# Optimization experiments

Hardware: AMD Instinct MI355X
Metric: run time of the kernel (lower is better)

## Reference

```python
import jax, jax.numpy as jnp
import numpy as np

B, D, K = 16384, 4096, 14
EPS = 1e-12  # torch F.normalize eps


def _normalize(x):
    n = jnp.sqrt(jnp.sum(x * x, axis=-1, keepdims=True))
    return x / jnp.maximum(n, EPS)


def setup_inputs() -> dict:
    key = jax.random.key(0)
    ks = jax.random.split(key, 9)
    image_feat = jax.random.normal(ks[0], (B, D), dtype=jnp.float32)
    text_feat = jax.random.normal(ks[1], (B, D), dtype=jnp.float32)
    disease_labels = jax.random.randint(ks[2], (B, K), 0, 2, dtype=jnp.int32)
    # nn.Linear default init: U(-1/sqrt(D), 1/sqrt(D))
    lim = 1.0 / np.sqrt(D)
    Wv = jax.random.uniform(ks[3], (D, D), jnp.float32, -lim, lim)
    bv = jax.random.uniform(ks[4], (D,), jnp.float32, -lim, lim)
    Wt = jax.random.uniform(ks[5], (D, D), jnp.float32, -lim, lim)
    bt = jax.random.uniform(ks[6], (D,), jnp.float32, -lim, lim)
    prototypes = jax.random.normal(ks[7], (K, D), dtype=jnp.float32) * 0.02
    cooccur = np.eye(K, dtype=np.float32)
    for i, j in [(1, 3), (0, 9), (7, 9)]:
        cooccur[i, j] = 0.7
        cooccur[j, i] = 0.7
    cooccurrence = jnp.asarray(cooccur)
    return {
        "image_feat": image_feat, "text_feat": text_feat,
        "disease_labels": disease_labels,
        "Wv": Wv, "bv": bv, "Wt": Wt, "bt": bt,
        "prototypes": prototypes, "cooccurrence": cooccurrence,
    }


def reference(image_feat, text_feat, disease_labels, Wv, bv, Wt, bt, prototypes, cooccurrence):
    labels_f = disease_labels.astype(jnp.float32)  # [B, K]
    v = _normalize(image_feat @ Wv.T + bv)          # [B, D]
    t = _normalize(text_feat @ Wt.T + bt)           # [B, D]
    p = _normalize(prototypes)                      # [K, D]
    v_sim = v @ p.T                                 # [B, K]
    t_sim = t @ p.T                                 # [B, K]
    # Coalition value is linear in the mask and the sampled coalitions differ
    # only at index i, so every Monte Carlo marginal equals this closed form
    # exactly (randomness cancels in value_with - value_without).
    shapley = 0.5 * (v_sim + t_sim) * labels_f      # [B, K]
    batch_cooccur = (labels_f.T @ labels_f) / labels_f.shape[0]  # [K, K]
    learned = jax.nn.sigmoid(cooccurrence)
    cooccur_loss = jnp.mean((learned - jax.lax.stop_gradient(batch_cooccur)) ** 2)
    return shapley, prototypes, cooccur_loss
```

## Files before the change

kernel.cpp:

```cpp
#include <hip/hip_runtime.h>

typedef __bf16 bf16x8 __attribute__((ext_vector_type(8)));
typedef float f32x4 __attribute__((ext_vector_type(4)));
typedef unsigned short u16;
typedef unsigned int u32;

#define D_DIM 4096
#define B_ROWS 16384
#define K_CLS 14
#define M_TOT 32768

__device__ __forceinline__ u32 f2bf(float f) {
    u32 u = __float_as_uint(f);
    return (u + 0x7FFFu + ((u >> 16) & 1u)) >> 16;
}
__device__ __forceinline__ float bfl(u32 u) { return __uint_as_float(u << 16); }
__device__ __forceinline__ float bfh(u32 u) { return __uint_as_float(u & 0xFFFF0000u); }

typedef __attribute__((address_space(3))) void lds_void;
typedef __attribute__((address_space(1))) void glb_void;

__device__ __forceinline__ void g2lds16(const void* g, void* l) {
    __builtin_amdgcn_global_load_lds(
        reinterpret_cast<glb_void*>(reinterpret_cast<uintptr_t>(g)),
        reinterpret_cast<lds_void*>(reinterpret_cast<uintptr_t>(l)),
        16, 0, 0);
}

__global__ void cast_bf16(const float* __restrict__ src, u16* __restrict__ dst, int n4) {
    int i = blockIdx.x * blockDim.x + threadIdx.x;
    int stride = gridDim.x * blockDim.x;
    for (; i < n4; i += stride) {
        float4 a = ((const float4*)src)[i];
        uint2 o;
        o.x = f2bf(a.x) | (f2bf(a.y) << 16);
        o.y = f2bf(a.z) | (f2bf(a.w) << 16);
        ((uint2*)dst)[i] = o;
    }
}

__global__ void proto_norm(const float* __restrict__ P, u16* __restrict__ pTbf,
                           float* __restrict__ outProto) {
    const int k = blockIdx.x;
    const int tid = threadIdx.x;
    float ss = 0.f;
    for (int d = tid; d < D_DIM; d += 256) {
        float v = P[k * D_DIM + d];
        ss += v * v;
    }
    for (int off = 32; off; off >>= 1) ss += __shfl_down(ss, off);
    __shared__ float red[4];
    if ((tid & 63) == 0) red[tid >> 6] = ss;
    __syncthreads();
    float tot = red[0] + red[1] + red[2] + red[3];
    float inv = 1.0f / fmaxf(sqrtf(tot), 1e-12f);
    for (int d = tid; d < D_DIM; d += 256) {
        float v = P[k * D_DIM + d];
        outProto[k * D_DIM + d] = v;
        pTbf[(size_t)d * 16 + k] = (u16)f2bf(v * inv);
    }
}

__global__ void cooccur_bc(const int* __restrict__ L, float* __restrict__ bc) {
    const int i = blockIdx.x / K_CLS, j = blockIdx.x % K_CLS;
    int s = 0;
    for (int b = threadIdx.x; b < B_ROWS; b += 256)
        s += L[b * K_CLS + i] * L[b * K_CLS + j];
    for (int off = 32; off; off >>= 1) s += __shfl_down(s, off);
    __shared__ int red[4];
    if ((threadIdx.x & 63) == 0) red[threadIdx.x >> 6] = s;
    __syncthreads();
    if (threadIdx.x == 0)
        bc[blockIdx.x] = (float)(red[0] + red[1] + red[2] + red[3]) / (float)B_ROWS;
}

__global__ void cooccur_loss(const float* __restrict__ C, const float* __restrict__ bc,
                             float* __restrict__ out) {
    const int t = threadIdx.x;
    float d2 = 0.f;
    if (t < K_CLS * K_CLS) {
        float s = 1.0f / (1.0f + expf(-C[t]));
        float d = s - bc[t];
        d2 = d * d;
    }
    for (int off = 32; off; off >>= 1) d2 += __shfl_down(d2, off);
    __shared__ float red[4];
    if ((t & 63) == 0) red[t >> 6] = d2;
    __syncthreads();
    if (t == 0) out[0] = (red[0] + red[1] + red[2] + red[3]) / (float)(K_CLS * K_CLS);
}

#define BK 64
#define NKT (D_DIM / BK)
#define TILE_E (256 * 64)

#define STAGE(ABUF, BBUF, k0) do {                                             \
    _Pragma("unroll")                                                          \
    for (int i_ = 0; i_ < 4; i_++)                                             \
        g2lds16(Apan + gOff[i_] + (k0), (ABUF) + lOff[i_]);                    \
    _Pragma("unroll")                                                          \
    for (int i_ = 0; i_ < 4; i_++)                                             \
        g2lds16(Bpan + gOff[i_] + (k0), (BBUF) + lOff[i_]);                    \
} while (0)

#define LOAD_B(BBUF) do {                                                      \
    _Pragma("unroll")                                                          \
    for (int ni_ = 0; ni_ < 4; ni_++) {                                        \
        bfr[ni_][0] = *(const bf16x8*)((BBUF) + bBase + ni_ * 16 * BK + so0);  \
        bfr[ni_][1] = *(const bf16x8*)((BBUF) + bBase + ni_ * 16 * BK + so1);  \
    }                                                                          \
} while (0)

#define LOAD_A(ABUF, q) do {                                                   \
    _Pragma("unroll")                                                          \
    for (int s_ = 0; s_ < 2; s_++) {                                           \
        afr[s_][0] = *(const bf16x8*)((ABUF) + aBase + ((q) * 32 + s_ * 16) * BK + so0); \
        afr[s_][1] = *(const bf16x8*)((ABUF) + aBase + ((q) * 32 + s_ * 16) * BK + so1); \
    }                                                                          \
} while (0)

#define MFMA_PHASE(q) do {                                                     \
    __builtin_amdgcn_s_setprio(1);                                             \
    _Pragma("unroll")                                                          \
    for (int s_ = 0; s_ < 2; s_++)                                             \
    _Pragma("unroll")                                                          \
    for (int ni_ = 0; ni_ < 4; ni_++) {                                        \
        acc[(q) * 2 + s_][ni_] = __builtin_amdgcn_mfma_f32_16x16x32_bf16(      \
            afr[s_][0], bfr[ni_][0], acc[(q) * 2 + s_][ni_], 0, 0, 0);         \
        acc[(q) * 2 + s_][ni_] = __builtin_amdgcn_mfma_f32_16x16x32_bf16(      \
            afr[s_][1], bfr[ni_][1], acc[(q) * 2 + s_][ni_], 0, 0, 0);         \
    }                                                                          \
    __builtin_amdgcn_s_setprio(0);                                             \
} while (0)

#define PHASE0(ABUF, BBUF) do { LOAD_B(BBUF); LOAD_A(ABUF, 0);                 \
    __builtin_amdgcn_s_barrier();                                              \
    asm volatile("s_waitcnt lgkmcnt(0)" ::: "memory");                         \
    __builtin_amdgcn_sched_barrier(0);                                         \
    MFMA_PHASE(0);                                                             \
    __builtin_amdgcn_s_barrier(); } while (0)

#define PHASEQ(ABUF, q) do { LOAD_A(ABUF, q);                                  \
    __builtin_amdgcn_s_barrier();                                              \
    asm volatile("s_waitcnt lgkmcnt(0)" ::: "memory");                         \
    __builtin_amdgcn_sched_barrier(0);                                         \
    MFMA_PHASE(q);                                                             \
    __builtin_amdgcn_s_barrier(); } while (0)

#define TILE_BODY(ABUF, BBUF, t) do {                                          \
    bf16x8 bfr[4][2], afr[2][2];                                               \
    PHASE0(ABUF, BBUF);                                                        \
    PHASEQ(ABUF, 1);                                                           \
    PHASEQ(ABUF, 2);                                                           \
    PHASEQ(ABUF, 3);                                                           \
    __builtin_amdgcn_sched_barrier(0);                                         \
    if ((t) + 2 < NKT) {                                                       \
        STAGE(ABUF, BBUF, ((t) + 2) * BK);                                     \
        asm volatile("s_waitcnt vmcnt(8)" ::: "memory");                       \
    } else if ((t) + 1 < NKT) {                                                \
        asm volatile("s_waitcnt vmcnt(0)" ::: "memory");                       \
    }                                                                          \
    __builtin_amdgcn_sched_barrier(0);                                         \
    __builtin_amdgcn_s_barrier();                                              \
} while (0)

__global__ __launch_bounds__(512, 2) void gemm_bt(
    const u16* __restrict__ Xbf,
    const u16* __restrict__ Wbf,
    const float* __restrict__ bv, const float* __restrict__ bt,
    u16* __restrict__ Ybf)
{
    __shared__ __align__(16) u16 lds[4 * TILE_E];
    u16* const As0 = lds;
    u16* const As1 = lds + TILE_E;
    u16* const Bs0 = lds + 2 * TILE_E;
    u16* const Bs1 = lds + 3 * TILE_E;

    const int tid = threadIdx.x;
    const int wave = tid >> 6, lane = tid & 63;

    const int bid = blockIdx.x;
    const int swzb = (bid & 7) * 256 + (bid >> 3);
    const int bn0 = (swzb & 15) * 256;
    const int bm0 = (swzb >> 4) * 256;
    const int half = (bm0 >= B_ROWS) ? 1 : 0;
    const u16* __restrict__ Apan = Xbf + (size_t)bm0 * D_DIM;
    const u16* __restrict__ Bpan = Wbf + (size_t)half * D_DIM * D_DIM
                                       + (size_t)bn0 * D_DIM;
    const float* bias = half ? bt : bv;

    const int lrow = lane >> 3;
    const int lslot = ((lane & 7) ^ lrow) * 8;
    size_t gOff[4];
    int lOff[4];
#pragma unroll
    for (int i = 0; i < 4; i++) {
        const int c = wave * 4 + i;
        gOff[i] = (size_t)(c * 8 + lrow) * D_DIM + lslot;
        lOff[i] = c * 512;
    }

    const int wm = wave >> 2, wn = wave & 3;
    const int mlane = lane & 15, quad = lane >> 4;
    const int lswz = lane & 7;
    const int so0 = (quad ^ lswz) * 8;
    const int so1 = ((4 + quad) ^ lswz) * 8;
    const int aBase = (wm * 128 + mlane) * BK;
    const int bBase = (wn * 64 + mlane) * BK;

    f32x4 acc[8][4] = {};

    STAGE(As0, Bs0, 0);
    STAGE(As1, Bs1, BK);
    asm volatile("s_waitcnt vmcnt(8)" ::: "memory");
    __builtin_amdgcn_sched_barrier(0);
    __builtin_amdgcn_s_barrier();

    for (int tt = 0; tt < NKT; tt += 2) {
        TILE_BODY(As0, Bs0, tt);
        TILE_BODY(As1, Bs1, tt + 1);
    }

#pragma unroll
    for (int ni = 0; ni < 4; ni++) {
        const int col = bn0 + wn * 64 + ni * 16 + mlane;
        const float bcol = bias[col];
#pragma unroll
        for (int mi = 0; mi < 8; mi++) {
            f32x4 v = acc[mi][ni];
            const size_t rb = (size_t)(bm0 + wm * 128 + mi * 16 + quad * 4) * D_DIM + col;
#pragma unroll
            for (int r = 0; r < 4; r++)
                Ybf[rb + (size_t)r * D_DIM] = (u16)f2bf(v[r] + bcol);
        }
    }
}

__global__ __launch_bounds__(256) void simproj(
    const u16* __restrict__ Ybf, const u16* __restrict__ pTbf,
    const int* __restrict__ L, float* __restrict__ out)
{
    const int tid = threadIdx.x;
    const int wave = tid >> 6, lane = tid & 63;
    const int r0 = blockIdx.x * 8 + wave * 2;
    const u16* Yi = Ybf + (size_t)r0 * D_DIM;
    const u16* Yt = Yi + (size_t)B_ROWS * D_DIM;

    float acc[4][15];
#pragma unroll
    for (int r = 0; r < 4; r++)
#pragma unroll
        for (int k = 0; k < 15; k++) acc[r][k] = 0.f;

#pragma unroll 2
    for (int i = 0; i < 64; i++) {
        const int d = lane + i * 64;
        const uint4* pq = (const uint4*)(pTbf + (size_t)d * 16);
        const uint4 q0 = pq[0], q1 = pq[1];
        const float p[14] = { bfl(q0.x), bfh(q0.x), bfl(q0.y), bfh(q0.y),
                              bfl(q0.z), bfh(q0.z), bfl(q0.w), bfh(q0.w),
                              bfl(q1.x), bfh(q1.x), bfl(q1.y), bfh(q1.y),
                              bfl(q1.z), bfh(q1.z) };
        float yv[4];
        yv[0] = bfl((u32)Yi[d]);
        yv[1] = bfl((u32)Yi[D_DIM + d]);
        yv[2] = bfl((u32)Yt[d]);
        yv[3] = bfl((u32)Yt[D_DIM + d]);
#pragma unroll
        for (int r = 0; r < 4; r++) {
            acc[r][14] += yv[r] * yv[r];
#pragma unroll
            for (int k = 0; k < 14; k++) acc[r][k] += yv[r] * p[k];
        }
    }
#pragma unroll
    for (int r = 0; r < 4; r++)
#pragma unroll
        for (int k = 0; k < 15; k++) {
            float v = acc[r][k];
            v += __shfl_xor(v, 1);  v += __shfl_xor(v, 2);  v += __shfl_xor(v, 4);
            v += __shfl_xor(v, 8);  v += __shfl_xor(v, 16); v += __shfl_xor(v, 32);
            acc[r][k] = v;
        }
    if (lane == 0) {
#pragma unroll
        for (int rr = 0; rr < 2; rr++) {
            const float iv = 1.0f / fmaxf(sqrtf(acc[rr][14]), 1e-12f);
            const float it = 1.0f / fmaxf(sqrtf(acc[2 + rr][14]), 1e-12f);
#pragma unroll
            for (int k = 0; k < 14; k++) {
                const int idx = (r0 + rr) * K_CLS + k;
                out[idx] = 0.5f * (acc[rr][k] * iv + acc[2 + rr][k] * it)
                           * (float)L[idx];
            }
        }
    }
}

extern "C" void kernel_launch(void* const* d_in, const int* in_sizes, int n_in,
                              void* d_out, int out_size, void* d_ws, size_t ws_size,
                              hipStream_t stream) {
    const float* image  = (const float*)d_in[0];
    const float* text   = (const float*)d_in[1];
    const int*   labels = (const int*)d_in[2];
    const float* Wv     = (const float*)d_in[3];
    const float* bv     = (const float*)d_in[4];
    const float* Wt     = (const float*)d_in[5];
    const float* bt     = (const float*)d_in[6];
    const float* protos = (const float*)d_in[7];
    const float* cooc   = (const float*)d_in[8];
    float* out = (float*)d_out;

    const size_t OFF_X   = 0;
    const size_t OFF_W   = 268435456ull;
    const size_t OFF_Y   = 335544320ull;
    const size_t OFF_PT  = 603979776ull;
    const size_t OFF_SIM = 604110848ull;
    const size_t OFF_BC  = 605945856ull;
    const size_t NEED    = 605946640ull;
    if (ws_size < NEED) return;
    (void)OFF_SIM;

    char* ws = (char*)d_ws;
    u16*   Xbf  = (u16*)(ws + OFF_X);
    u16*   Wbf  = (u16*)(ws + OFF_W);
    u16*   Ybf  = (u16*)(ws + OFF_Y);
    u16*   pTbf = (u16*)(ws + OFF_PT);
    float* bc   = (float*)(ws + OFF_BC);

    cast_bf16<<<4096, 256, 0, stream>>>(image, Xbf, (B_ROWS * D_DIM) / 4);
    cast_bf16<<<4096, 256, 0, stream>>>(text, Xbf + (size_t)B_ROWS * D_DIM, (B_ROWS * D_DIM) / 4);
    cast_bf16<<<2048, 256, 0, stream>>>(Wv, Wbf, (D_DIM * D_DIM) / 4);
    cast_bf16<<<2048, 256, 0, stream>>>(Wt, Wbf + (size_t)D_DIM * D_DIM, (D_DIM * D_DIM) / 4);

    proto_norm<<<K_CLS, 256, 0, stream>>>(protos, pTbf, out + B_ROWS * K_CLS);
    cooccur_bc<<<K_CLS * K_CLS, 256, 0, stream>>>(labels, bc);
    cooccur_loss<<<1, 256, 0, stream>>>(cooc, bc, out + B_ROWS * K_CLS + K_CLS * D_DIM);

    gemm_bt<<<(M_TOT / 256) * (D_DIM / 256), 512, 0, stream>>>(Xbf, Wbf, bv, bt, Ybf);

    simproj<<<B_ROWS / 8, 256, 0, stream>>>(Ybf, pTbf, labels, out);
}
```

Measured before the change: 1.888 ms.

## Interleave half-tile staging into GEMM phases, remap blocks, merge casts, widen simproj

The GEMM now issues half-tile global-to-LDS loads inside each MFMA phase, spreading the prefetch across the loop instead of doing one block per tile. The wave-to-row mapping and the XCD block mapping change so that each XCD covers contiguous M panels. The four cast launches become a single kernel, and simproj loads 8-wide vectors for 4 rows per wave to reuse each prototype load across more rows. These changes cut launch overhead and idle time waiting on loads, at the cost of more register pressure in simproj and more delicate vmcnt accounting.

```diff
diff --git a/kernel.cpp b/kernel.cpp
--- a/kernel.cpp
+++ b/kernel.cpp
@@ -27,15 +27,25 @@
         16, 0, 0);
 }
 
-__global__ void cast_bf16(const float* __restrict__ src, u16* __restrict__ dst, int n4) {
+__global__ void cast_all(const float* __restrict__ im, const float* __restrict__ tx,
+                         const float* __restrict__ wv, const float* __restrict__ wt,
+                         u16* __restrict__ Xbf, u16* __restrict__ Wbf) {
+    const int nX = (B_ROWS * D_DIM) / 4;
+    const int nW = (D_DIM * D_DIM) / 4;
+    const int total = 2 * nX + 2 * nW;
     int i = blockIdx.x * blockDim.x + threadIdx.x;
-    int stride = gridDim.x * blockDim.x;
-    for (; i < n4; i += stride) {
-        float4 a = ((const float4*)src)[i];
+    const int stride = gridDim.x * blockDim.x;
+    for (; i < total; i += stride) {
+        const float* s; u16* d; int off;
+        if (i < nX)               { s = im; d = Xbf;                       off = i; }
+        else if (i < 2 * nX)      { s = tx; d = Xbf + (size_t)nX * 4;      off = i - nX; }
+        else if (i < 2 * nX + nW) { s = wv; d = Wbf;                       off = i - 2 * nX; }
+        else                      { s = wt; d = Wbf + (size_t)nW * 4;      off = i - 2 * nX - nW; }
+        float4 a = ((const float4*)s)[off];
         uint2 o;
         o.x = f2bf(a.x) | (f2bf(a.y) << 16);
         o.y = f2bf(a.z) | (f2bf(a.w) << 16);
-        ((uint2*)dst)[i] = o;
+        ((uint2*)d)[off] = o;
     }
 }
 
@@ -94,28 +104,28 @@
 #define NKT (D_DIM / BK)
 #define TILE_E (256 * 64)
 
-#define STAGE(ABUF, BBUF, k0) do {                                             \
-    _Pragma("unroll")                                                          \
-    for (int i_ = 0; i_ < 4; i_++)                                             \
-        g2lds16(Apan + gOff[i_] + (k0), (ABUF) + lOff[i_]);                    \
-    _Pragma("unroll")                                                          \
-    for (int i_ = 0; i_ < 4; i_++)                                             \
-        g2lds16(Bpan + gOff[i_] + (k0), (BBUF) + lOff[i_]);                    \
-} while (0)
-
-#define LOAD_B(BBUF) do {                                                      \
+#define STAGE_HALF(DST, PAN, k0, h) do {                                       \
+    _Pragma("unroll")                                                          \
+    for (int i_ = 0; i_ < 2; i_++) {                                           \
+        const int c_ = (h) * 16 + wave * 2 + i_;                               \
+        g2lds16((PAN) + (size_t)(c_ * 8 + lrow) * D_DIM + lslot + (k0),        \
+                (DST) + c_ * 512);                                             \
+    }                                                                          \
+} while (0)
+
+#define LOAD_B(BR) do {                                                        \
     _Pragma("unroll")                                                          \
     for (int ni_ = 0; ni_ < 4; ni_++) {                                        \
-        bfr[ni_][0] = *(const bf16x8*)((BBUF) + bBase + ni_ * 16 * BK + so0);  \
-        bfr[ni_][1] = *(const bf16x8*)((BBUF) + bBase + ni_ * 16 * BK + so1);  \
+        bfr[ni_][0] = *(const bf16x8*)((BR) + bBase + ni_ * 16 * BK + so0);    \
+        bfr[ni_][1] = *(const bf16x8*)((BR) + bBase + ni_ * 16 * BK + so1);    \
     }                                                                          \
 } while (0)
 
-#define LOAD_A(ABUF, q) do {                                                   \
+#define LOAD_A(AR, q) do {                                                     \
     _Pragma("unroll")                                                          \
     for (int s_ = 0; s_ < 2; s_++) {                                           \
-        afr[s_][0] = *(const bf16x8*)((ABUF) + aBase + ((q) * 32 + s_ * 16) * BK + so0); \
-        afr[s_][1] = *(const bf16x8*)((ABUF) + aBase + ((q) * 32 + s_ * 16) * BK + so1); \
+        afr[s_][0] = *(const bf16x8*)((AR) + aBase + ((q) * 64 + s_ * 16) * BK + so0); \
+        afr[s_][1] = *(const bf16x8*)((AR) + aBase + ((q) * 64 + s_ * 16) * BK + so1); \
     }                                                                          \
 } while (0)
 
@@ -133,36 +143,20 @@
     __builtin_amdgcn_s_setprio(0);                                             \
 } while (0)
 
-#define PHASE0(ABUF, BBUF) do { LOAD_B(BBUF); LOAD_A(ABUF, 0);                 \
-    __builtin_amdgcn_s_barrier();                                              \
-    asm volatile("s_waitcnt lgkmcnt(0)" ::: "memory");                         \
+#define PHASE(AR, BR, q, WITHB, STAGE_STMT, TAIL_STMT) do {                    \
+    if (WITHB) { LOAD_B(BR); }                                                 \
+    LOAD_A(AR, q);                                                             \
+    STAGE_STMT;                                                                \
     __builtin_amdgcn_sched_barrier(0);                                         \
-    MFMA_PHASE(0);                                                             \
-    __builtin_amdgcn_s_barrier(); } while (0)
-
-#define PHASEQ(ABUF, q) do { LOAD_A(ABUF, q);                                  \
     __builtin_amdgcn_s_barrier();                                              \
     asm volatile("s_waitcnt lgkmcnt(0)" ::: "memory");                         \
     __builtin_amdgcn_sched_barrier(0);                                         \
     MFMA_PHASE(q);                                                             \
-    __builtin_amdgcn_s_barrier(); } while (0)
-
-#define TILE_BODY(ABUF, BBUF, t) do {                                          \
-    bf16x8 bfr[4][2], afr[2][2];                                               \
-    PHASE0(ABUF, BBUF);                                                        \
-    PHASEQ(ABUF, 1);                                                           \
-    PHASEQ(ABUF, 2);                                                           \
-    PHASEQ(ABUF, 3);                                                           \
-    __builtin_amdgcn_sched_barrier(0);                                         \
-    if ((t) + 2 < NKT) {                                                       \
-        STAGE(ABUF, BBUF, ((t) + 2) * BK);                                     \
-        asm volatile("s_waitcnt vmcnt(8)" ::: "memory");                       \
-    } else if ((t) + 1 < NKT) {                                                \
-        asm volatile("s_waitcnt vmcnt(0)" ::: "memory");                       \
-    }                                                                          \
-    __builtin_amdgcn_sched_barrier(0);                                         \
+    TAIL_STMT;                                                                 \
     __builtin_amdgcn_s_barrier();                                              \
 } while (0)
+
+#define WAIT2 asm volatile("s_waitcnt vmcnt(2)" ::: "memory")
 
 __global__ __launch_bounds__(512, 2) void gemm_bt(
     const u16* __restrict__ Xbf,
@@ -180,9 +174,9 @@
     const int wave = tid >> 6, lane = tid & 63;
 
     const int bid = blockIdx.x;
-    const int swzb = (bid & 7) * 256 + (bid >> 3);
-    const int bn0 = (swzb & 15) * 256;
-    const int bm0 = (swzb >> 4) * 256;
+    const int xcd = bid & 7, loc = bid >> 3;
+    const int bn0 = (loc >> 4) * 256;
+    const int bm0 = (xcd * 16 + (loc & 15)) * 256;
     const int half = (bm0 >= B_ROWS) ? 1 : 0;
     const u16* __restrict__ Apan = Xbf + (size_t)bm0 * D_DIM;
     const u16* __restrict__ Bpan = Wbf + (size_t)half * D_DIM * D_DIM
@@ -191,35 +185,41 @@
 
     const int lrow = lane >> 3;
     const int lslot = ((lane & 7) ^ lrow) * 8;
-    size_t gOff[4];
-    int lOff[4];
-#pragma unroll
-    for (int i = 0; i < 4; i++) {
-        const int c = wave * 4 + i;
-        gOff[i] = (size_t)(c * 8 + lrow) * D_DIM + lslot;
-        lOff[i] = c * 512;
-    }
 
     const int wm = wave >> 2, wn = wave & 3;
     const int mlane = lane & 15, quad = lane >> 4;
     const int lswz = lane & 7;
     const int so0 = (quad ^ lswz) * 8;
     const int so1 = ((4 + quad) ^ lswz) * 8;
-    const int aBase = (wm * 128 + mlane) * BK;
+    const int aBase = (wm * 32 + mlane) * BK;
     const int bBase = (wn * 64 + mlane) * BK;
 
     f32x4 acc[8][4] = {};
 
-    STAGE(As0, Bs0, 0);
-    STAGE(As1, Bs1, BK);
-    asm volatile("s_waitcnt vmcnt(8)" ::: "memory");
+    STAGE_HALF(As0, Apan, 0, 0);
+    STAGE_HALF(As0, Apan, 0, 1);
+    STAGE_HALF(Bs0, Bpan, 0, 0);
+    STAGE_HALF(Bs0, Bpan, 0, 1);
+    STAGE_HALF(As1, Apan, BK, 0);
+    WAIT2;
     __builtin_amdgcn_sched_barrier(0);
     __builtin_amdgcn_s_barrier();
 
     for (int tt = 0; tt < NKT; tt += 2) {
-        TILE_BODY(As0, Bs0, tt);
-        TILE_BODY(As1, Bs1, tt + 1);
-    }
+        const int k1 = (tt + 1) * BK;
+        const int k2 = (tt + 2) * BK;
+        const int k3 = (tt + 3) * BK;
+        bf16x8 bfr[4][2], afr[2][2];
+        PHASE(As0, Bs0, 0, 1, STAGE_HALF(As1, Apan, k1, 1), );
+        PHASE(As0, Bs0, 1, 0, STAGE_HALF(Bs1, Bpan, k1, 0), );
+        PHASE(As0, Bs0, 2, 0, STAGE_HALF(Bs1, Bpan, k1, 1), );
+        PHASE(As0, Bs0, 3, 0, STAGE_HALF(As0, Apan, k2, 0), WAIT2);
+        PHASE(As1, Bs1, 0, 1, STAGE_HALF(As0, Apan, k2, 1), );
+        PHASE(As1, Bs1, 1, 0, STAGE_HALF(Bs0, Bpan, k2, 0), );
+        PHASE(As1, Bs1, 2, 0, STAGE_HALF(Bs0, Bpan, k2, 1), );
+        PHASE(As1, Bs1, 3, 0, STAGE_HALF(As1, Apan, k3, 0), WAIT2);
+    }
+    asm volatile("s_waitcnt vmcnt(0)" ::: "memory");
 
 #pragma unroll
     for (int ni = 0; ni < 4; ni++) {
@@ -228,7 +228,8 @@
 #pragma unroll
         for (int mi = 0; mi < 8; mi++) {
             f32x4 v = acc[mi][ni];
-            const size_t rb = (size_t)(bm0 + wm * 128 + mi * 16 + quad * 4) * D_DIM + col;
+            const int row0 = bm0 + (mi >> 1) * 64 + wm * 32 + (mi & 1) * 16 + quad * 4;
+            const size_t rb = (size_t)row0 * D_DIM + col;
 #pragma unroll
             for (int r = 0; r < 4; r++)
                 Ybf[rb + (size_t)r * D_DIM] = (u16)f2bf(v[r] + bcol);
@@ -242,39 +243,43 @@
 {
     const int tid = threadIdx.x;
     const int wave = tid >> 6, lane = tid & 63;
-    const int r0 = blockIdx.x * 8 + wave * 2;
+    const int r0 = blockIdx.x * 16 + wave * 4;
     const u16* Yi = Ybf + (size_t)r0 * D_DIM;
     const u16* Yt = Yi + (size_t)B_ROWS * D_DIM;
 
-    float acc[4][15];
-#pragma unroll
-    for (int r = 0; r < 4; r++)
+    float acc[8][15];
+#pragma unroll
+    for (int r = 0; r < 8; r++)
 #pragma unroll
         for (int k = 0; k < 15; k++) acc[r][k] = 0.f;
 
-#pragma unroll 2
-    for (int i = 0; i < 64; i++) {
-        const int d = lane + i * 64;
-        const uint4* pq = (const uint4*)(pTbf + (size_t)d * 16);
-        const uint4 q0 = pq[0], q1 = pq[1];
-        const float p[14] = { bfl(q0.x), bfh(q0.x), bfl(q0.y), bfh(q0.y),
-                              bfl(q0.z), bfh(q0.z), bfl(q0.w), bfh(q0.w),
-                              bfl(q1.x), bfh(q1.x), bfl(q1.y), bfh(q1.y),
-                              bfl(q1.z), bfh(q1.z) };
-        float yv[4];
-        yv[0] = bfl((u32)Yi[d]);
-        yv[1] = bfl((u32)Yi[D_DIM + d]);
-        yv[2] = bfl((u32)Yt[d]);
-        yv[3] = bfl((u32)Yt[D_DIM + d]);
+    for (int i = 0; i < 8; i++) {
+        const int d0 = i * 512 + lane * 8;
+        bf16x8 yv[8];
 #pragma unroll
         for (int r = 0; r < 4; r++) {
-            acc[r][14] += yv[r] * yv[r];
-#pragma unroll
-            for (int k = 0; k < 14; k++) acc[r][k] += yv[r] * p[k];
-        }
-    }
-#pragma unroll
-    for (int r = 0; r < 4; r++)
+            yv[r]     = *(const bf16x8*)(Yi + (size_t)r * D_DIM + d0);
+            yv[4 + r] = *(const bf16x8*)(Yt + (size_t)r * D_DIM + d0);
+        }
+#pragma unroll
+        for (int j = 0; j < 8; j++) {
+            const uint4* pq = (const uint4*)(pTbf + (size_t)(d0 + j) * 16);
+            const uint4 q0 = pq[0], q1 = pq[1];
+            const float p[14] = { bfl(q0.x), bfh(q0.x), bfl(q0.y), bfh(q0.y),
+                                  bfl(q0.z), bfh(q0.z), bfl(q0.w), bfh(q0.w),
+                                  bfl(q1.x), bfh(q1.x), bfl(q1.y), bfh(q1.y),
+                                  bfl(q1.z), bfh(q1.z) };
+#pragma unroll
+            for (int r = 0; r < 8; r++) {
+                const float y = (float)yv[r][j];
+                acc[r][14] += y * y;
+#pragma unroll
+                for (int k = 0; k < 14; k++) acc[r][k] += y * p[k];
+            }
+        }
+    }
+#pragma unroll
+    for (int r = 0; r < 8; r++)
 #pragma unroll
         for (int k = 0; k < 15; k++) {
             float v = acc[r][k];
@@ -284,13 +289,13 @@
         }
     if (lane == 0) {
 #pragma unroll
-        for (int rr = 0; rr < 2; rr++) {
+        for (int rr = 0; rr < 4; rr++) {
             const float iv = 1.0f / fmaxf(sqrtf(acc[rr][14]), 1e-12f);
-            const float it = 1.0f / fmaxf(sqrtf(acc[2 + rr][14]), 1e-12f);
+            const float it = 1.0f / fmaxf(sqrtf(acc[4 + rr][14]), 1e-12f);
 #pragma unroll
             for (int k = 0; k < 14; k++) {
                 const int idx = (r0 + rr) * K_CLS + k;
-                out[idx] = 0.5f * (acc[rr][k] * iv + acc[2 + rr][k] * it)
+                out[idx] = 0.5f * (acc[rr][k] * iv + acc[4 + rr][k] * it)
                            * (float)L[idx];
             }
         }
@@ -315,11 +320,9 @@
     const size_t OFF_W   = 268435456ull;
     const size_t OFF_Y   = 335544320ull;
     const size_t OFF_PT  = 603979776ull;
-    const size_t OFF_SIM = 604110848ull;
     const size_t OFF_BC  = 605945856ull;
     const size_t NEED    = 605946640ull;
     if (ws_size < NEED) return;
-    (void)OFF_SIM;
 
     char* ws = (char*)d_ws;
     u16*   Xbf  = (u16*)(ws + OFF_X);
@@ -328,10 +331,7 @@
     u16*   pTbf = (u16*)(ws + OFF_PT);
     float* bc   = (float*)(ws + OFF_BC);
 
-    cast_bf16<<<4096, 256, 0, stream>>>(image, Xbf, (B_ROWS * D_DIM) / 4);
-    cast_bf16<<<4096, 256, 0, stream>>>(text, Xbf + (size_t)B_ROWS * D_DIM, (B_ROWS * D_DIM) / 4);
-    cast_bf16<<<2048, 256, 0, stream>>>(Wv, Wbf, (D_DIM * D_DIM) / 4);
-    cast_bf16<<<2048, 256, 0, stream>>>(Wt, Wbf + (size_t)D_DIM * D_DIM, (D_DIM * D_DIM) / 4);
+    cast_all<<<4096, 256, 0, stream>>>(image, text, Wv, Wt, Xbf, Wbf);
 
     proto_norm<<<K_CLS, 256, 0, stream>>>(protos, pTbf, out + B_ROWS * K_CLS);
     cooccur_bc<<<K_CLS * K_CLS, 256, 0, stream>>>(labels, bc);
@@ -339,5 +339,5 @@
 
     gemm_bt<<<(M_TOT / 256) * (D_DIM / 256), 512, 0, stream>>>(Xbf, Wbf, bv, bt, Ybf);
 
-    simproj<<<B_ROWS / 8, 256, 0, stream>>>(Ybf, pTbf, labels, out);
-}
+    simproj<<<B_ROWS / 16, 256, 0, stream>>>(Ybf, pTbf, labels, out);
+}
```

New measurement: 1.832 ms. 3.0% less time.
